# Performance work log

Measured on AMD Instinct MI355X. Metric: run time of the kernel, lower is better.

The kernel has to match this reference:

```python
import jax, jax.numpy as jnp
import numpy as np

B, S, D, H = 2, 2048, 1024, 16
DK = D // H


def setup_inputs() -> dict:
    key = jax.random.key(0)
    ks = jax.random.split(key, 13)
    scale = 1.0 / np.sqrt(D)
    return {
        "query": jax.random.normal(ks[0], (B, S, D), jnp.float32),
        "key": jax.random.normal(ks[1], (B, S, D), jnp.float32),
        "value": jax.random.normal(ks[2], (B, S, D), jnp.float32),
        "mask": jax.random.randint(ks[3], (B, S, S), 0, 2, jnp.int32),
        "Wq": jax.random.normal(ks[4], (D, D), jnp.float32) * scale,
        "bq": jnp.zeros((D,), jnp.float32),
        "Wk": jax.random.normal(ks[5], (D, D), jnp.float32) * scale,
        "bk": jnp.zeros((D,), jnp.float32),
        "Wv": jax.random.normal(ks[6], (D, D), jnp.float32) * scale,
        "bv": jnp.zeros((D,), jnp.float32),
        "Wo": jax.random.normal(ks[7], (D, D), jnp.float32) * scale,
        "bo": jnp.zeros((D,), jnp.float32),
    }


def _split_heads(x):
    # [B,S,D] -> [B,H,S,DK]
    b, s, _ = x.shape
    return x.reshape(b, s, H, DK).transpose(0, 2, 1, 3)


def reference(query, key, value, mask, Wq, bq, Wk, bk, Wv, bv, Wo, bo):
    q = _split_heads(query @ Wq + bq)
    k = _split_heads(key @ Wk + bk)
    v = _split_heads(value @ Wv + bv)
    # scaled dot-product scores [B,H,Sq,Sk]
    scores = jnp.einsum("bhqd,bhkd->bhqk", q, k) / jnp.sqrt(jnp.float32(DK))
    scores = jnp.where(mask[:, None, :, :] == 0, jnp.float32(-1e9), scores)
    p_attn = jax.nn.softmax(scores, axis=-1)  # dropout p=0.0 -> identity
    x = jnp.einsum("bhqk,bhkd->bhqd", p_attn, v)
    x = x.transpose(0, 2, 1, 3).reshape(query.shape[0], -1, D)
    return x @ Wo + bo
```

## Files before the change

kernel.cpp:

```cpp
#include <hip/hip_runtime.h>
#include <cstdint>

#define B_ 2
#define S_ 2048
#define D_ 1024
#define H_ 16
#define DK_ 64
#define SCALE_ 0.18033688011112042f

typedef float f32x4 __attribute__((ext_vector_type(4)));
typedef float f32x16 __attribute__((ext_vector_type(16)));
typedef __bf16 bf16x8 __attribute__((ext_vector_type(8)));
typedef unsigned short u16x8 __attribute__((ext_vector_type(8)));
typedef unsigned short u16x4 __attribute__((ext_vector_type(4)));
typedef unsigned int u32x4 __attribute__((ext_vector_type(4)));

__device__ __forceinline__ unsigned short f2bf(float x) {
  unsigned int u = __builtin_bit_cast(unsigned int, x);
  u += 0x7FFFu + ((u >> 16) & 1u);
  return (unsigned short)(u >> 16);
}

__device__ __forceinline__ void gload16(const void* g, void* l) {
  __builtin_amdgcn_global_load_lds((__attribute__((address_space(1))) void*)(void*)g,
                                   (__attribute__((address_space(3))) void*)l, 16, 0, 0);
}

__device__ __forceinline__ float exp2v(float x) {
  float r;
  asm("v_exp_f32 %0, %1" : "=v"(r) : "v"(x));
  return r;
}

__device__ __forceinline__ unsigned int cvtpk(float a, float b) {
  unsigned int r;
  asm("v_cvt_pk_bf16_f32 %0, %1, %2" : "=v"(r) : "v"(a), "v"(b));
  return r;
}

__device__ __forceinline__ unsigned int bit_mask(unsigned int w, int bit) {
#if __has_builtin(__builtin_amdgcn_sbfe)
  return (unsigned int)__builtin_amdgcn_sbfe((int)w, bit, 1);
#else
  return (unsigned int)((int)(w << (31 - bit)) >> 31);
#endif
}

__global__ __launch_bounds__(256) void prep_kernel(
    const float* __restrict__ q, const float* __restrict__ k, const float* __restrict__ v,
    unsigned short* __restrict__ oq, unsigned short* __restrict__ ok,
    unsigned short* __restrict__ ov,
    const float* __restrict__ w0, const float* __restrict__ w1,
    const float* __restrict__ w2, const float* __restrict__ w3,
    unsigned short* o0, unsigned short* o1, unsigned short* o2, unsigned short* o3,
    const int* __restrict__ mask, unsigned int* __restrict__ mb) {
  __shared__ float t[32][33];
  const int bid = blockIdx.x;
  const int tid = threadIdx.x;
  if (bid < 6144) {
    const int z = bid >> 11, vb = bid & 2047;
    const float* in = z == 0 ? q : z == 1 ? k : v;
    unsigned short* out = z == 0 ? oq : z == 1 ? ok : ov;
    const int n = B_ * S_ * D_;
    int idx = vb * 256 + tid;
#pragma unroll
    for (int i = idx * 4; i < n; i += 2048 * 256 * 4) {
      f32x4 vv = *(const f32x4*)(in + i);
      u16x4 o;
#pragma unroll
      for (int j = 0; j < 4; ++j) o[j] = f2bf(vv[j]);
      *(u16x4*)(out + i) = o;
    }
  } else if (bid < 10240) {
    const int r = bid - 6144;
    const int z = r >> 10, rr = r & 1023;
    const float* W;
    unsigned short* O;
    float sc = 1.f;
    if (z == 0) { W = w0; O = o0; sc = SCALE_; }
    else if (z == 1) { W = w1; O = o1; }
    else if (z == 2) { W = w2; O = o2; }
    else { W = w3; O = o3; }
    const int n0 = (rr & 31) * 32, k0 = (rr >> 5) * 32;
    const int tx = tid & 31, ty = tid >> 5;
    for (int i = ty; i < 32; i += 8) t[i][tx] = W[(size_t)(k0 + i) * D_ + n0 + tx];
    __syncthreads();
    for (int i = ty; i < 32; i += 8) O[(size_t)(n0 + i) * D_ + k0 + tx] = f2bf(t[tx][i] * sc);
  } else {
    const int wid = ((bid - 10240) << 2) + (tid >> 6);
    const int lane = tid & 63;
    size_t base = (size_t)wid << 6;
    unsigned long long bits = __ballot(mask[base + lane] != 0);
    if (lane == 0) *(unsigned long long*)(mb + (base >> 5)) = bits;
  }
}

template <int MODE>
__device__ __forceinline__ void gemm128(const unsigned short* __restrict__ A,
                                        const unsigned short* __restrict__ BT,
                                        const float* __restrict__ bias, float bsc,
                                        void* __restrict__ Cp, int M, int N, int K) {
  __shared__ unsigned short Al[128 * 32];
  __shared__ unsigned short Bl[128 * 32];
  const int tid = threadIdx.x;
  const int lane = tid & 63;
  const int w = tid >> 6;
  const int wr = w >> 1, wc = w & 1;
  const int wg = blockIdx.x + gridDim.x * blockIdx.y;
  const int work = (wg & 7) * 32 + (wg >> 3);
  const int nx = N >> 7;
  const int m0 = (work / nx) * 128, n0 = (work % nx) * 128;

  f32x4 acc[4][4] = {};
  const int nk = K / 32;
  const int srow = lane >> 2;
  const int scol = (lane & 3) * 8;

  const int fr = lane & 15;
  const int fc = (lane >> 4) * 8;

  for (int kt = 0; kt < nk; ++kt) {
    __syncthreads();
#pragma unroll
    for (int it = 0; it < 2; ++it) {
      int chunk = it * 4 + w;
      const unsigned short* ga = A + (size_t)(m0 + chunk * 16 + srow) * K + kt * 32 + scol;
      gload16(ga, &Al[chunk * 512]);
      const unsigned short* gb = BT + (size_t)(n0 + chunk * 16 + srow) * K + kt * 32 + scol;
      gload16(gb, &Bl[chunk * 512]);
    }
    __syncthreads();
    bf16x8 af[4], bf[4];
#pragma unroll
    for (int i = 0; i < 4; ++i)
      af[i] = __builtin_bit_cast(bf16x8, *(const u16x8*)&Al[(wr * 64 + i * 16 + fr) * 32 + fc]);
#pragma unroll
    for (int j = 0; j < 4; ++j)
      bf[j] = __builtin_bit_cast(bf16x8, *(const u16x8*)&Bl[(wc * 64 + j * 16 + fr) * 32 + fc]);
    __builtin_amdgcn_s_setprio(1);
#pragma unroll
    for (int i = 0; i < 4; ++i)
#pragma unroll
      for (int j = 0; j < 4; ++j)
        acc[i][j] = __builtin_amdgcn_mfma_f32_16x16x32_bf16(af[i], bf[j], acc[i][j], 0, 0, 0);
    __builtin_amdgcn_s_setprio(0);
  }

  const int rg = (lane >> 4) * 4;
  const int cg = lane & 15;
#pragma unroll
  for (int i = 0; i < 4; ++i)
#pragma unroll
    for (int j = 0; j < 4; ++j) {
      int col = n0 + wc * 64 + j * 16 + cg;
      float bv = bias[col] * bsc;
#pragma unroll
      for (int e = 0; e < 4; ++e) {
        int row = m0 + wr * 64 + i * 16 + rg + e;
        float v = acc[i][j][e] + bv;
        if (MODE == 1)
          ((float*)Cp)[(size_t)row * N + col] = v;
        else if (MODE == 0)
          ((unsigned short*)Cp)[(size_t)row * N + col] = f2bf(v);
        else
          ((unsigned short*)Cp)[((size_t)(row >> 11) * D_ + col) * S_ + (row & (S_ - 1))] = f2bf(v);
      }
    }
}

__global__ __launch_bounds__(256) void qkv_gemm_kernel(
    const unsigned short* __restrict__ xq, const unsigned short* __restrict__ xk,
    const unsigned short* __restrict__ xv, const unsigned short* __restrict__ wtq,
    const unsigned short* __restrict__ wtk, const unsigned short* __restrict__ wtv,
    const float* __restrict__ bq, const float* __restrict__ bk, const float* __restrict__ bv,
    unsigned short* q, unsigned short* k, unsigned short* vt) {
  if (blockIdx.z == 0)
    gemm128<0>(xq, wtq, bq, SCALE_, (void*)q, B_ * S_, D_, D_);
  else if (blockIdx.z == 1)
    gemm128<0>(xk, wtk, bk, 1.f, (void*)k, B_ * S_, D_, D_);
  else
    gemm128<2>(xv, wtv, bv, 1.f, (void*)vt, B_ * S_, D_, D_);
}

__global__ __launch_bounds__(256) void out_gemm_kernel(const unsigned short* __restrict__ x,
                                                       const unsigned short* __restrict__ wto,
                                                       const float* __restrict__ bo,
                                                       float* __restrict__ out) {
  gemm128<1>(x, wto, bo, 1.f, (void*)out, B_ * S_, D_, D_);
}

__global__ __launch_bounds__(256, 2) void attn_kernel(const unsigned short* __restrict__ Q,
                                                      const unsigned short* __restrict__ K,
                                                      const unsigned short* __restrict__ Vt,
                                                      const unsigned int* __restrict__ mb,
                                                      unsigned short* __restrict__ X) {
  __shared__ unsigned short Kl[2][128 * 64];
  __shared__ unsigned short Vl[2][2][64 * 64];

  const int tid = threadIdx.x;
  const int lane = tid & 63;
  const int w = tid >> 6;
  const int ql = lane & 31;
  const int hi = lane >> 5;

  const int wg = blockIdx.x + gridDim.x * blockIdx.y;
  const int swz = (wg & 7) * 64 + (wg >> 3);
  const int qt = swz & 15;
  const int bh = swz >> 4;
  const int b = bh >> 4, h = bh & 15;
  const int q_g = qt * 128 + w * 32 + ql;

  const size_t qkbase = ((size_t)b * S_) * D_ + h * DK_;
  const size_t vtbase = ((size_t)b * D_ + h * DK_) * S_;

  bf16x8 qf[4];
  {
    const unsigned short* qp = Q + qkbase + (size_t)q_g * D_ + hi * 8;
#pragma unroll
    for (int c = 0; c < 4; ++c)
      qf[c] = __builtin_bit_cast(bf16x8, *(const u16x8*)(qp + c * 16));
  }

  const int lr = lane >> 3;
  const int seg = (lane & 7) ^ lr;
  const unsigned short* Ks = K + qkbase + (size_t)(w * 32 + lr) * D_ + seg * 8;
  const unsigned short* Vs = Vt + vtbase + (size_t)(w * 16 + lr) * S_ + seg * 8;

  auto stage = [&](int kt, int bufi) {
#pragma unroll
    for (int c = 0; c < 4; ++c)
      gload16(Ks + ((size_t)kt * 128 + c * 8) * D_, &Kl[bufi][(w * 32 + c * 8) * 64]);
#pragma unroll
    for (int c = 0; c < 4; ++c)
      gload16(Vs + (size_t)((c & 1) * 8) * S_ + kt * 128 + (c >> 1) * 64,
              &Vl[bufi][c >> 1][(w * 16 + (c & 1) * 8) * 64]);
  };

  const unsigned long long* mrow =
      (const unsigned long long*)mb + ((size_t)b * S_ + q_g) * 32;

  f32x16 o0 = {}, o1 = {};
  f32x16 o2 = {};
  const int sw = (ql & 7) << 4;

  const unsigned int one2 = 0x3F803F80u;
  const bf16x8 onesf = __builtin_bit_cast(bf16x8, u32x4{one2, one2, one2, one2});

  stage(0, 0);
  const int NT = S_ / 128;

  for (int kt = 0; kt < NT; ++kt) {
    const int buf = kt & 1;
    __syncthreads();
    unsigned long long M0 = mrow[kt * 2], M1 = mrow[kt * 2 + 1];

    bf16x8 kf[2][2][4];
#pragma unroll
    for (int hh = 0; hh < 2; ++hh) {
      const char* Kb = (const char*)&Kl[buf][hh * 64 * 64];
#pragma unroll
      for (int r = 0; r < 2; ++r)
#pragma unroll
        for (int c = 0; c < 4; ++c)
          kf[hh][r][c] = __builtin_bit_cast(
              bf16x8, *(const u16x8*)(Kb + (((r * 32 + ql) * 128 + c * 32 + hi * 16) ^ sw)));
    }
    if (kt < NT - 1) stage(kt + 1, buf ^ 1);

    f32x16 s[2][2] = {};
    __builtin_amdgcn_s_setprio(1);
#pragma unroll
    for (int hh = 0; hh < 2; ++hh)
#pragma unroll
      for (int c = 0; c < 4; ++c) {
        s[hh][0] = __builtin_amdgcn_mfma_f32_32x32x16_bf16(kf[hh][0][c], qf[c], s[hh][0], 0, 0, 0);
        s[hh][1] = __builtin_amdgcn_mfma_f32_32x32x16_bf16(kf[hh][1][c], qf[c], s[hh][1], 0, 0, 0);
      }
    __builtin_amdgcn_s_setprio(0);

    bf16x8 vf[2][2][4];
#pragma unroll
    for (int hh = 0; hh < 2; ++hh) {
      const char* Vb = (const char*)&Vl[buf][hh][0];
#pragma unroll
      for (int nt = 0; nt < 2; ++nt)
#pragma unroll
        for (int kc = 0; kc < 4; ++kc)
          vf[hh][nt][kc] = __builtin_bit_cast(
              bf16x8, *(const u16x8*)(Vb + (((nt * 32 + ql) * 128 + kc * 32 + hi * 16) ^ sw)));
    }

    u32x4 pw[2][4];
#pragma unroll
    for (int hh = 0; hh < 2; ++hh) {
      const unsigned long long M = hh ? M1 : M0;
      unsigned int W0 = (unsigned int)(M >> (hi * 4));
      unsigned int W1 = (unsigned int)(M >> (32 + hi * 4));
#pragma unroll
      for (int r = 0; r < 16; ++r) {
        const int krl = (r & 3) + 8 * (r >> 2);
        unsigned int mk0 = bit_mask(W0, krl);
        float p0 = exp2v(s[hh][0][r]);
        s[hh][0][r] = __builtin_bit_cast(float, __builtin_bit_cast(unsigned int, p0) & mk0);
        unsigned int mk1 = bit_mask(W1, krl);
        float p1 = exp2v(s[hh][1][r]);
        s[hh][1][r] = __builtin_bit_cast(float, __builtin_bit_cast(unsigned int, p1) & mk1);
      }
#pragma unroll
      for (int kc = 0; kc < 4; ++kc) {
        const int rb = (kc & 1) * 8;
        const int st = kc >> 1;
        unsigned int w0 = cvtpk(s[hh][st][rb + 0], s[hh][st][rb + 1]);
        unsigned int w1 = cvtpk(s[hh][st][rb + 2], s[hh][st][rb + 3]);
        unsigned int w2 = cvtpk(s[hh][st][rb + 4], s[hh][st][rb + 5]);
        unsigned int w3 = cvtpk(s[hh][st][rb + 6], s[hh][st][rb + 7]);
        unsigned int u0, u1, u2, u3;
#if __has_builtin(__builtin_amdgcn_permlane32_swap)
        { auto r02 = __builtin_amdgcn_permlane32_swap(w0, w2, false, false);
          u0 = r02[0]; u2 = r02[1]; }
        { auto r13 = __builtin_amdgcn_permlane32_swap(w1, w3, false, false);
          u1 = r13[0]; u3 = r13[1]; }
#else
        { unsigned int t0 = (unsigned int)__shfl_xor((int)w0, 32);
          unsigned int t2 = (unsigned int)__shfl_xor((int)w2, 32);
          u0 = hi ? t2 : w0; u2 = hi ? w2 : t0;
          unsigned int t1 = (unsigned int)__shfl_xor((int)w1, 32);
          unsigned int t3 = (unsigned int)__shfl_xor((int)w3, 32);
          u1 = hi ? t3 : w1; u3 = hi ? w3 : t1; }
#endif
        pw[hh][kc] = u32x4{u0, u1, u2, u3};
      }
    }

    __builtin_amdgcn_s_setprio(1);
#pragma unroll
    for (int hh = 0; hh < 2; ++hh)
#pragma unroll
      for (int kc = 0; kc < 4; ++kc) {
        bf16x8 pf = __builtin_bit_cast(bf16x8, pw[hh][kc]);
        o0 = __builtin_amdgcn_mfma_f32_32x32x16_bf16(vf[hh][0][kc], pf, o0, 0, 0, 0);
        o1 = __builtin_amdgcn_mfma_f32_32x32x16_bf16(vf[hh][1][kc], pf, o1, 0, 0, 0);
        o2 = __builtin_amdgcn_mfma_f32_32x32x16_bf16(onesf, pf, o2, 0, 0, 0);
      }
    __builtin_amdgcn_s_setprio(0);
  }

  float inv = 1.f / o2[0];
  unsigned short* Xp = X + ((size_t)b * S_ + q_g) * D_ + h * DK_;
#pragma unroll
  for (int rb = 0; rb < 4; ++rb) {
    int d0 = 8 * rb + 4 * hi;
    *(unsigned int*)(Xp + d0) = cvtpk(o0[4 * rb + 0] * inv, o0[4 * rb + 1] * inv);
    *(unsigned int*)(Xp + d0 + 2) = cvtpk(o0[4 * rb + 2] * inv, o0[4 * rb + 3] * inv);
    *(unsigned int*)(Xp + 32 + d0) = cvtpk(o1[4 * rb + 0] * inv, o1[4 * rb + 1] * inv);
    *(unsigned int*)(Xp + 32 + d0 + 2) = cvtpk(o1[4 * rb + 2] * inv, o1[4 * rb + 3] * inv);
  }
}

extern "C" void kernel_launch(void* const* d_in, const int* in_sizes, int n_in,
                              void* d_out, int out_size, void* d_ws, size_t ws_size,
                              hipStream_t stream) {
  const float* query = (const float*)d_in[0];
  const float* key = (const float*)d_in[1];
  const float* value = (const float*)d_in[2];
  const int* mask = (const int*)d_in[3];
  const float* Wq = (const float*)d_in[4];
  const float* bq = (const float*)d_in[5];
  const float* Wk = (const float*)d_in[6];
  const float* bk = (const float*)d_in[7];
  const float* Wv = (const float*)d_in[8];
  const float* bv = (const float*)d_in[9];
  const float* Wo = (const float*)d_in[10];
  const float* bo = (const float*)d_in[11];
  float* out = (float*)d_out;

  const size_t ACT = (size_t)B_ * S_ * D_;
  const size_t WSZ = (size_t)D_ * D_;
  unsigned short* ws = (unsigned short*)d_ws;
  unsigned short* xq = ws;
  unsigned short* xk = xq + ACT;
  unsigned short* xv = xk + ACT;
  unsigned short* wtq = xv + ACT;
  unsigned short* wtk = wtq + WSZ;
  unsigned short* wtv = wtk + WSZ;
  unsigned short* wto = wtv + WSZ;
  unsigned short* qb = wto + WSZ;
  unsigned short* kb = qb + ACT;
  unsigned short* vt = kb + ACT;
  unsigned int* mbp = (unsigned int*)(vt + ACT);
  unsigned short* xb = xq;

  prep_kernel<<<43008, 256, 0, stream>>>(query, key, value, xq, xk, xv,
                                         Wq, Wk, Wv, Wo, wtq, wtk, wtv, wto,
                                         mask, mbp);

  dim3 gg(8, 32, 3);
  qkv_gemm_kernel<<<gg, 256, 0, stream>>>(xq, xk, xv, wtq, wtk, wtv, bq, bk, bv, qb, kb, vt);

  dim3 ag(S_ / 128, B_ * H_);
  attn_kernel<<<ag, 256, 0, stream>>>(qb, kb, vt, mbp, xb);

  dim3 og(8, 32, 1);
  out_gemm_kernel<<<og, 256, 0, stream>>>(xb, wto, bo, out);
}
```

Measured before the change: 163.6 us.

## Double-buffer GEMM LDS tiles, swizzle LDS layout, narrow output GEMM tiles

The GEMM helper now stages its A and B tiles into two LDS buffers, so the next k-tile's global-to-LDS loads are issued while the current tile feeds the MFMAs, and one barrier per iteration is dropped. The LDS column index is XOR-swizzled on both write and read to cut bank conflicts on fragment loads. The output projection switches to 128x64 tiles with four warps stacked along M and twice as many workgroups, to fill more CUs. The cost is double the LDS footprint and slightly more address arithmetic.

```diff
diff --git a/kernel.cpp b/kernel.cpp
--- a/kernel.cpp
+++ b/kernel.cpp
@@ -95,53 +95,69 @@
   }
 }
 
-template <int MODE>
-__device__ __forceinline__ void gemm128(const unsigned short* __restrict__ A,
-                                        const unsigned short* __restrict__ BT,
-                                        const float* __restrict__ bias, float bsc,
-                                        void* __restrict__ Cp, int M, int N, int K) {
-  __shared__ unsigned short Al[128 * 32];
-  __shared__ unsigned short Bl[128 * 32];
+template <int MODE, int TN, int NWN>
+__device__ __forceinline__ void gemm_t(const unsigned short* __restrict__ A,
+                                       const unsigned short* __restrict__ BT,
+                                       const float* __restrict__ bias, float bsc,
+                                       void* __restrict__ Cp, int M, int N, int K) {
+  constexpr int NWM = 4 / NWN;
+  constexpr int WM = 128 / NWM;
+  constexpr int WN = TN / NWN;
+  constexpr int MR = WM / 16, NR = WN / 16;
+  __shared__ unsigned short Al[2][128 * 32];
+  __shared__ unsigned short Bl[2][TN * 32];
   const int tid = threadIdx.x;
   const int lane = tid & 63;
   const int w = tid >> 6;
-  const int wr = w >> 1, wc = w & 1;
+  const int wr = w / NWN, wc = w % NWN;
+  const int nwg = gridDim.x * gridDim.y;
   const int wg = blockIdx.x + gridDim.x * blockIdx.y;
-  const int work = (wg & 7) * 32 + (wg >> 3);
-  const int nx = N >> 7;
-  const int m0 = (work / nx) * 128, n0 = (work % nx) * 128;
-
-  f32x4 acc[4][4] = {};
+  const int work = (wg & 7) * (nwg >> 3) + (wg >> 3);
+  const int nx = N / TN;
+  const int m0 = (work / nx) * 128, n0 = (work % nx) * TN;
+
+  f32x4 acc[MR][NR] = {};
   const int nk = K / 32;
   const int srow = lane >> 2;
-  const int scol = (lane & 3) * 8;
+  const int scol = ((lane & 3) ^ ((lane >> 3) & 3)) * 8;
 
   const int fr = lane & 15;
-  const int fc = (lane >> 4) * 8;
-
-  for (int kt = 0; kt < nk; ++kt) {
-    __syncthreads();
+  const int rsw = ((lane >> 4) ^ ((fr >> 1) & 3)) * 8;
+
+  auto stage = [&](int kt, int bufi) {
 #pragma unroll
     for (int it = 0; it < 2; ++it) {
       int chunk = it * 4 + w;
-      const unsigned short* ga = A + (size_t)(m0 + chunk * 16 + srow) * K + kt * 32 + scol;
-      gload16(ga, &Al[chunk * 512]);
-      const unsigned short* gb = BT + (size_t)(n0 + chunk * 16 + srow) * K + kt * 32 + scol;
-      gload16(gb, &Bl[chunk * 512]);
-    }
+      gload16(A + (size_t)(m0 + chunk * 16 + srow) * K + kt * 32 + scol,
+              &Al[bufi][chunk * 512]);
+    }
+#pragma unroll
+    for (int it = 0; it < TN / 64; ++it) {
+      int chunk = it * 4 + w;
+      gload16(BT + (size_t)(n0 + chunk * 16 + srow) * K + kt * 32 + scol,
+              &Bl[bufi][chunk * 512]);
+    }
+  };
+
+  stage(0, 0);
+  for (int kt = 0; kt < nk; ++kt) {
+    const int buf = kt & 1;
     __syncthreads();
-    bf16x8 af[4], bf[4];
-#pragma unroll
-    for (int i = 0; i < 4; ++i)
-      af[i] = __builtin_bit_cast(bf16x8, *(const u16x8*)&Al[(wr * 64 + i * 16 + fr) * 32 + fc]);
-#pragma unroll
-    for (int j = 0; j < 4; ++j)
-      bf[j] = __builtin_bit_cast(bf16x8, *(const u16x8*)&Bl[(wc * 64 + j * 16 + fr) * 32 + fc]);
+    if (kt + 1 < nk) stage(kt + 1, buf ^ 1);
+    bf16x8 af[MR], bf[NR];
+#pragma unroll
+    for (int i = 0; i < MR; ++i)
+      af[i] = __builtin_bit_cast(bf16x8,
+          *(const u16x8*)&Al[buf][(wr * WM + i * 16 + fr) * 32 + rsw]);
+#pragma unroll
+    for (int j = 0; j < NR; ++j)
+      bf[j] = __builtin_bit_cast(bf16x8,
+          *(const u16x8*)&Bl[buf][(wc * WN + j * 16 + fr) * 32 + rsw]);
     __builtin_amdgcn_s_setprio(1);
 #pragma unroll
-    for (int i = 0; i < 4; ++i)
-#pragma unroll
-      for (int j = 0; j < 4; ++j)
+    for (int i = 0; i < MR; ++i)
+#pragma unroll
+      for (int j = 0; j < NR; ++j)
         acc[i][j] = __builtin_amdgcn_mfma_f32_16x16x32_bf16(af[i], bf[j], acc[i][j], 0, 0, 0);
     __builtin_amdgcn_s_setprio(0);
   }
@@ -149,14 +165,14 @@
   const int rg = (lane >> 4) * 4;
   const int cg = lane & 15;
 #pragma unroll
-  for (int i = 0; i < 4; ++i)
-#pragma unroll
-    for (int j = 0; j < 4; ++j) {
-      int col = n0 + wc * 64 + j * 16 + cg;
+  for (int i = 0; i < MR; ++i)
+#pragma unroll
+    for (int j = 0; j < NR; ++j) {
+      int col = n0 + wc * WN + j * 16 + cg;
       float bv = bias[col] * bsc;
 #pragma unroll
       for (int e = 0; e < 4; ++e) {
-        int row = m0 + wr * 64 + i * 16 + rg + e;
+        int row = m0 + wr * WM + i * 16 + rg + e;
         float v = acc[i][j][e] + bv;
         if (MODE == 1)
           ((float*)Cp)[(size_t)row * N + col] = v;
@@ -175,18 +191,18 @@
     const float* __restrict__ bq, const float* __restrict__ bk, const float* __restrict__ bv,
     unsigned short* q, unsigned short* k, unsigned short* vt) {
   if (blockIdx.z == 0)
-    gemm128<0>(xq, wtq, bq, SCALE_, (void*)q, B_ * S_, D_, D_);
+    gemm_t<0, 128, 2>(xq, wtq, bq, SCALE_, (void*)q, B_ * S_, D_, D_);
   else if (blockIdx.z == 1)
-    gemm128<0>(xk, wtk, bk, 1.f, (void*)k, B_ * S_, D_, D_);
+    gemm_t<0, 128, 2>(xk, wtk, bk, 1.f, (void*)k, B_ * S_, D_, D_);
   else
-    gemm128<2>(xv, wtv, bv, 1.f, (void*)vt, B_ * S_, D_, D_);
+    gemm_t<2, 128, 2>(xv, wtv, bv, 1.f, (void*)vt, B_ * S_, D_, D_);
 }
 
 __global__ __launch_bounds__(256) void out_gemm_kernel(const unsigned short* __restrict__ x,
                                                        const unsigned short* __restrict__ wto,
                                                        const float* __restrict__ bo,
                                                        float* __restrict__ out) {
-  gemm128<1>(x, wto, bo, 1.f, (void*)out, B_ * S_, D_, D_);
+  gemm_t<1, 64, 1>(x, wto, bo, 1.f, (void*)out, B_ * S_, D_, D_);
 }
 
 __global__ __launch_bounds__(256, 2) void attn_kernel(const unsigned short* __restrict__ Q,
@@ -400,6 +416,6 @@
   dim3 ag(S_ / 128, B_ * H_);
   attn_kernel<<<ag, 256, 0, stream>>>(qb, kb, vt, mbp, xb);
 
-  dim3 og(8, 32, 1);
+  dim3 og(16, 32, 1);
   out_gemm_kernel<<<og, 256, 0, stream>>>(xb, wto, bo, out);
 }
```

After: 153.7 us. 6.0% less time.
